# Kernel optimization log

Measured on AMD Instinct MI355X. Metric: run time of the kernel, lower is better.

The kernel has to match this reference:

```python
import jax, jax.numpy as jnp
import numpy as np

EPS = 1e-5
DIM = 1024

def layer_norm(x, gamma, beta):
    mu = jnp.mean(x, axis=-1, keepdims=True)
    var = jnp.var(x, axis=-1, keepdims=True)
    return (x - mu) * jax.lax.rsqrt(var + EPS) * gamma + beta

def setup_inputs() -> dict:
    key = jax.random.key(0)
    k1, k2 = jax.random.split(key)
    return {
        "image_features": jax.random.normal(k1, (32, 1024, DIM), dtype=jnp.float32),
        "text_features": jax.random.normal(k2, (32, 512, DIM), dtype=jnp.float32),
        "gamma": jnp.ones((DIM,), dtype=jnp.float32),
        "beta": jnp.zeros((DIM,), dtype=jnp.float32),
    }

def reference(image_features, text_features, gamma, beta):
    scale = DIM ** (-0.5)
    image_norm = layer_norm(image_features, gamma, beta)   # [B, Ni, D]
    text_norm = layer_norm(text_features, gamma, beta)     # [B, Nt, D]
    # shared attention matrix, softmax only over text axis
    attn = jax.nn.softmax(jnp.einsum('bid,btd->bit', image_norm, text_norm) * scale, axis=-1)  # [B, Ni, Nt]
    image_attended = jnp.einsum('bit,btd->bid', attn, text_norm)   # [B, Ni, D]
    text_attended = jnp.einsum('bit,bid->btd', attn, image_norm)   # [B, Nt, D] (attn reused transposed, no re-softmax)
    return (image_features + image_attended, text_features + text_attended)
```

## Files before the change

### kernel.cpp

```cpp
#include <hip/hip_runtime.h>
#include <hip/hip_bf16.h>

#define B_  32
#define NI_ 1024
#define NT_ 512
#define D_  1024

typedef __attribute__((ext_vector_type(8))) short bf16x8;
typedef __attribute__((ext_vector_type(4))) float f32x4;

__device__ __forceinline__ ushort f2b(float f) {
  unsigned u = __builtin_bit_cast(unsigned, f);
  u = (u + 0x7FFFu + ((u >> 16) & 1u)) >> 16;
  return (ushort)u;
}

__global__ __launch_bounds__(256) void ln_bf16_kernel(
    const float* __restrict__ x, const float* __restrict__ gamma,
    const float* __restrict__ beta, ushort* __restrict__ out)
{
  const int row  = blockIdx.x * 4 + (threadIdx.x >> 6);
  const int lane = threadIdx.x & 63;
  const float* xr = x + (size_t)row * D_;
  float4 v[4];
  float s = 0.f, sq = 0.f;
#pragma unroll
  for (int q = 0; q < 4; ++q) {
    v[q] = *reinterpret_cast<const float4*>(xr + q * 256 + lane * 4);
    s  += v[q].x + v[q].y + v[q].z + v[q].w;
    sq += v[q].x*v[q].x + v[q].y*v[q].y + v[q].z*v[q].z + v[q].w*v[q].w;
  }
#pragma unroll
  for (int m = 1; m < 64; m <<= 1) {
    s  += __shfl_xor(s,  m);
    sq += __shfl_xor(sq, m);
  }
  const float mean = s * (1.f / D_);
  const float rstd = rsqrtf(sq * (1.f / D_) - mean * mean + 1e-5f);
  ushort* orow = out + (size_t)row * D_;
#pragma unroll
  for (int q = 0; q < 4; ++q) {
    const float4 g  = *reinterpret_cast<const float4*>(gamma + q * 256 + lane * 4);
    const float4 bt = *reinterpret_cast<const float4*>(beta  + q * 256 + lane * 4);
    ushort4 o;
    o.x = f2b((v[q].x - mean) * rstd * g.x + bt.x);
    o.y = f2b((v[q].y - mean) * rstd * g.y + bt.y);
    o.z = f2b((v[q].z - mean) * rstd * g.z + bt.z);
    o.w = f2b((v[q].w - mean) * rstd * g.w + bt.w);
    *reinterpret_cast<ushort4*>(orow + q * 256 + lane * 4) = o;
  }
}

__global__ __launch_bounds__(256) void transpose_bf16_kernel(
    const ushort* __restrict__ in, ushort* __restrict__ out, int R, int C)
{
  __shared__ ushort lds[64][68];
  const size_t nb = (size_t)blockIdx.z * (size_t)R * C;
  const ushort* ib = in + nb;
  ushort* ob = out + nb;
  const int c0 = blockIdx.x * 64, r0 = blockIdx.y * 64;
  const int t = threadIdx.x;
#pragma unroll
  for (int it = 0; it < 2; ++it) {
    const int r = (t >> 3) + 32 * it;
    const int c = (t & 7) * 8;
    uint4 val = *reinterpret_cast<const uint4*>(ib + (size_t)(r0 + r) * C + c0 + c);
    *reinterpret_cast<uint2*>(&lds[r][c])     = make_uint2(val.x, val.y);
    *reinterpret_cast<uint2*>(&lds[r][c + 4]) = make_uint2(val.z, val.w);
  }
  __syncthreads();
#pragma unroll
  for (int it = 0; it < 2; ++it) {
    const int c  = (t >> 3) + 32 * it;
    const int rb = (t & 7) * 8;
    union { ushort u[8]; uint4 v; } pk;
#pragma unroll
    for (int j = 0; j < 8; ++j) pk.u[j] = lds[rb + j][c];
    *reinterpret_cast<uint4*>(ob + (size_t)(c0 + c) * R + r0 + rb) = pk.v;
  }
}

__global__ __launch_bounds__(512) void qk_softmax_kernel(
    const ushort* __restrict__ qn,
    const ushort* __restrict__ kn,
    ushort* __restrict__ attn_it,
    ushort* __restrict__ attn_ti)
{
  __shared__ __align__(16) ushort Asm[2][64 * 32];
  __shared__ __align__(16) ushort Bsm[2][512 * 32];
  __shared__ __align__(16) float redm[64][8];
  __shared__ __align__(16) float reds[64][8];

  const int bid = blockIdx.x;
  const int sid = (bid & 7) * 64 + (bid >> 3);
  const int b   = sid >> 4;
  const int i0  = (sid & 15) * 64;
  const int tid  = threadIdx.x;
  const int w    = tid >> 6;
  const int lane = tid & 63;
  const int lr   = lane & 15;
  const int g    = lane >> 4;

  const ushort* qb = qn + ((size_t)b * NI_ + i0) * D_;
  const ushort* kb = kn + (size_t)b * NT_ * D_;

  const int srow = tid >> 2;
  const int scol = (tid & 3) * 8;

  uint4 ra, rb0, rb1, rb2, rb3;
  auto LOAD = [&](int t) {
    const int ko = t * 32 + scol;
    if (tid < 256) ra = *reinterpret_cast<const uint4*>(qb + (size_t)srow * D_ + ko);
    rb0 = *reinterpret_cast<const uint4*>(kb + (size_t)(srow      ) * D_ + ko);
    rb1 = *reinterpret_cast<const uint4*>(kb + (size_t)(srow + 128) * D_ + ko);
    rb2 = *reinterpret_cast<const uint4*>(kb + (size_t)(srow + 256) * D_ + ko);
    rb3 = *reinterpret_cast<const uint4*>(kb + (size_t)(srow + 384) * D_ + ko);
  };
  auto WRITE = [&](int nb) {
    if (tid < 256) *reinterpret_cast<uint4*>(&Asm[nb][tid * 8]) = ra;
    *reinterpret_cast<uint4*>(&Bsm[nb][tid * 8        ]) = rb0;
    *reinterpret_cast<uint4*>(&Bsm[nb][tid * 8 +  4096]) = rb1;
    *reinterpret_cast<uint4*>(&Bsm[nb][tid * 8 +  8192]) = rb2;
    *reinterpret_cast<uint4*>(&Bsm[nb][tid * 8 + 12288]) = rb3;
  };

  f32x4 acc[4][4];
#pragma unroll
  for (int i = 0; i < 4; ++i)
#pragma unroll
    for (int j = 0; j < 4; ++j) acc[i][j] = (f32x4){0.f, 0.f, 0.f, 0.f};

  LOAD(0); WRITE(0); __syncthreads();
  const int nst = D_ / 32;
  int cur = 0;
  for (int t = 0; t < nst; ++t) {
    if (t + 1 < nst) LOAD(t + 1);
    const ushort* As = Asm[cur];
    const ushort* Bs = Bsm[cur];
    bf16x8 af[4], bf[4];
#pragma unroll
    for (int i = 0; i < 4; ++i)
      af[i] = *reinterpret_cast<const bf16x8*>(As + i * 512 + lr * 32 + g * 8);
#pragma unroll
    for (int j = 0; j < 4; ++j)
      bf[j] = *reinterpret_cast<const bf16x8*>(Bs + w * 2048 + j * 512 + lr * 32 + g * 8);
#pragma unroll
    for (int i = 0; i < 4; ++i)
#pragma unroll
      for (int j = 0; j < 4; ++j)
        acc[i][j] = __builtin_amdgcn_mfma_f32_16x16x32_bf16(af[i], bf[j], acc[i][j], 0, 0, 0);
    __syncthreads();
    if (t + 1 < nst) WRITE(cur ^ 1);
    __syncthreads();
    cur ^= 1;
  }

  const float c1 = 0.03125f * 1.44269504f;

  float mx[4][4];
#pragma unroll
  for (int i = 0; i < 4; ++i)
#pragma unroll
    for (int r = 0; r < 4; ++r) {
      float m = fmaxf(fmaxf(acc[i][0][r], acc[i][1][r]),
                      fmaxf(acc[i][2][r], acc[i][3][r]));
      m = fmaxf(m, __shfl_xor(m, 1));
      m = fmaxf(m, __shfl_xor(m, 2));
      m = fmaxf(m, __shfl_xor(m, 4));
      m = fmaxf(m, __shfl_xor(m, 8));
      mx[i][r] = m;
    }
  if (lr == 0) {
#pragma unroll
    for (int i = 0; i < 4; ++i)
#pragma unroll
      for (int r = 0; r < 4; ++r) redm[i * 16 + g * 4 + r][w] = mx[i][r];
  }
  __syncthreads();
  float gm[4][4];
#pragma unroll
  for (int i = 0; i < 4; ++i)
#pragma unroll
    for (int r = 0; r < 4; ++r) {
      const int row = i * 16 + g * 4 + r;
      const float4 a0 = *reinterpret_cast<const float4*>(&redm[row][0]);
      const float4 a1 = *reinterpret_cast<const float4*>(&redm[row][4]);
      gm[i][r] = fmaxf(fmaxf(fmaxf(a0.x, a0.y), fmaxf(a0.z, a0.w)),
                       fmaxf(fmaxf(a1.x, a1.y), fmaxf(a1.z, a1.w)));
    }

  float sm[4][4];
#pragma unroll
  for (int i = 0; i < 4; ++i)
#pragma unroll
    for (int r = 0; r < 4; ++r) sm[i][r] = 0.f;
#pragma unroll
  for (int i = 0; i < 4; ++i)
#pragma unroll
    for (int j = 0; j < 4; ++j)
#pragma unroll
      for (int r = 0; r < 4; ++r) {
        const float p = exp2f((acc[i][j][r] - gm[i][r]) * c1);
        acc[i][j][r] = p;
        sm[i][r] += p;
      }
#pragma unroll
  for (int i = 0; i < 4; ++i)
#pragma unroll
    for (int r = 0; r < 4; ++r) {
      float s = sm[i][r];
      s += __shfl_xor(s, 1);
      s += __shfl_xor(s, 2);
      s += __shfl_xor(s, 4);
      s += __shfl_xor(s, 8);
      sm[i][r] = s;
    }
  if (lr == 0) {
#pragma unroll
    for (int i = 0; i < 4; ++i)
#pragma unroll
      for (int r = 0; r < 4; ++r) reds[i * 16 + g * 4 + r][w] = sm[i][r];
  }
  __syncthreads();
  float inv[4][4];
#pragma unroll
  for (int i = 0; i < 4; ++i)
#pragma unroll
    for (int r = 0; r < 4; ++r) {
      const int row = i * 16 + g * 4 + r;
      const float4 a0 = *reinterpret_cast<const float4*>(&reds[row][0]);
      const float4 a1 = *reinterpret_cast<const float4*>(&reds[row][4]);
      inv[i][r] = 1.f / (a0.x + a0.y + a0.z + a0.w + a1.x + a1.y + a1.z + a1.w);
    }

#pragma unroll
  for (int i = 0; i < 4; ++i) {
    const int rbase = i0 + i * 16 + g * 4;
#pragma unroll
    for (int j = 0; j < 4; ++j) {
      const int tcol = w * 64 + j * 16 + lr;
      ushort4 pk;
      pk.x = f2b(acc[i][j][0] * inv[i][0]);
      pk.y = f2b(acc[i][j][1] * inv[i][1]);
      pk.z = f2b(acc[i][j][2] * inv[i][2]);
      pk.w = f2b(acc[i][j][3] * inv[i][3]);
      ushort* it_p = attn_it + ((size_t)b * NI_ + rbase) * NT_ + tcol;
      it_p[0 * NT_] = pk.x;
      it_p[1 * NT_] = pk.y;
      it_p[2 * NT_] = pk.z;
      it_p[3 * NT_] = pk.w;
      *reinterpret_cast<ushort4*>(attn_ti + ((size_t)b * NT_ + tcol) * NI_ + rbase) = pk;
    }
  }
}

__global__ __launch_bounds__(256) void bt_gemm_add_kernel(
    const ushort* __restrict__ A,
    const ushort* __restrict__ Bm,
    const float* __restrict__ add,
    float* __restrict__ out,
    int M, int N, int K)
{
  __shared__ __align__(16) ushort Asm[2][128 * 32];
  __shared__ __align__(16) ushort Bsm[2][128 * 32];

  const int b    = blockIdx.z;
  const int m0   = blockIdx.y * 128;
  const int n0   = blockIdx.x * 128;
  const int tid  = threadIdx.x;
  const int w    = tid >> 6;
  const int lane = tid & 63;
  const int lr   = lane & 15;
  const int g    = lane >> 4;
  const int wm   = (w >> 1) * 64;
  const int wn   = (w & 1) * 64;

  const ushort* Ab = A  + ((size_t)b * M + m0) * K;
  const ushort* Bb = Bm + ((size_t)b * N + n0) * K;

  const int srow = tid >> 2;
  const int scol = (tid & 3) * 8;

  uint4 ra0, ra1, rbx0, rbx1;
  auto LOAD = [&](int t) {
    const int ko = t * 32 + scol;
    ra0  = *reinterpret_cast<const uint4*>(Ab + (size_t)(srow     ) * K + ko);
    ra1  = *reinterpret_cast<const uint4*>(Ab + (size_t)(srow + 64) * K + ko);
    rbx0 = *reinterpret_cast<const uint4*>(Bb + (size_t)(srow     ) * K + ko);
    rbx1 = *reinterpret_cast<const uint4*>(Bb + (size_t)(srow + 64) * K + ko);
  };
  auto WRITE = [&](int nb) {
    *reinterpret_cast<uint4*>(&Asm[nb][tid * 8       ]) = ra0;
    *reinterpret_cast<uint4*>(&Asm[nb][tid * 8 + 2048]) = ra1;
    *reinterpret_cast<uint4*>(&Bsm[nb][tid * 8       ]) = rbx0;
    *reinterpret_cast<uint4*>(&Bsm[nb][tid * 8 + 2048]) = rbx1;
  };

  f32x4 acc[4][4];
#pragma unroll
  for (int i = 0; i < 4; ++i)
#pragma unroll
    for (int j = 0; j < 4; ++j) acc[i][j] = (f32x4){0.f, 0.f, 0.f, 0.f};

  LOAD(0); WRITE(0); __syncthreads();
  const int nst = K / 32;
  int cur = 0;
  for (int t = 0; t < nst; ++t) {
    if (t + 1 < nst) LOAD(t + 1);
    const ushort* As = Asm[cur];
    const ushort* Bs = Bsm[cur];
    bf16x8 af[4], bf[4];
#pragma unroll
    for (int i = 0; i < 4; ++i)
      af[i] = *reinterpret_cast<const bf16x8*>(As + (wm + i * 16 + lr) * 32 + g * 8);
#pragma unroll
    for (int j = 0; j < 4; ++j)
      bf[j] = *reinterpret_cast<const bf16x8*>(Bs + (wn + j * 16 + lr) * 32 + g * 8);
#pragma unroll
    for (int i = 0; i < 4; ++i)
#pragma unroll
      for (int j = 0; j < 4; ++j)
        acc[i][j] = __builtin_amdgcn_mfma_f32_16x16x32_bf16(af[i], bf[j], acc[i][j], 0, 0, 0);
    __syncthreads();
    if (t + 1 < nst) WRITE(cur ^ 1);
    __syncthreads();
    cur ^= 1;
  }

  const size_t ob = (size_t)b * M * N;
  const int rbase = m0 + wm + g * 4;
#pragma unroll
  for (int i = 0; i < 4; ++i)
#pragma unroll
    for (int j = 0; j < 4; ++j) {
      const int c = n0 + wn + j * 16 + lr;
#pragma unroll
      for (int r = 0; r < 4; ++r) {
        const size_t idx = ob + (size_t)(rbase + i * 16 + r) * N + c;
        out[idx] = add[idx] + acc[i][j][r];
      }
    }
}

extern "C" void kernel_launch(void* const* d_in, const int* in_sizes, int n_in,
                              void* d_out, int out_size, void* d_ws, size_t ws_size,
                              hipStream_t stream) {
  const float* imgf  = (const float*)d_in[0];
  const float* txtf  = (const float*)d_in[1];
  const float* gamma = (const float*)d_in[2];
  const float* beta  = (const float*)d_in[3];

  float* out0 = (float*)d_out;
  float* out1 = out0 + (size_t)B_ * NI_ * D_;

  const size_t SZ = (size_t)B_ * NT_ * NI_ * 2;
  char* ws = (char*)d_ws;
  ushort* attn_ti = (ushort*)ws;
  ushort* attn_it = (ushort*)(ws + SZ);
  ushort* txnT    = (ushort*)(ws + 2 * SZ);
  ushort* imnT    = (ushort*)(ws + SZ);
  ushort* imn     = (ushort*)out1;
  ushort* txn     = (ushort*)out0;

  ln_bf16_kernel<<<(B_ * NI_) / 4, 256, 0, stream>>>(imgf, gamma, beta, imn);
  ln_bf16_kernel<<<(B_ * NT_) / 4, 256, 0, stream>>>(txtf, gamma, beta, txn);
  qk_softmax_kernel<<<(NI_ / 64) * B_, 512, 0, stream>>>(imn, txn, attn_it, attn_ti);
  transpose_bf16_kernel<<<dim3(D_ / 64, NT_ / 64, B_), 256, 0, stream>>>(txn, txnT, NT_, D_);
  bt_gemm_add_kernel<<<dim3(D_ / 128, NI_ / 128, B_), 256, 0, stream>>>(
      attn_it, txnT, imgf, out0, NI_, D_, NT_);
  transpose_bf16_kernel<<<dim3(D_ / 64, NI_ / 64, B_), 256, 0, stream>>>(imn, imnT, NI_, D_);
  bt_gemm_add_kernel<<<dim3(D_ / 128, NT_ / 128, B_), 256, 0, stream>>>(
      attn_ti, imnT, txtf, out1, NT_, D_, NI_);
}
```

Baseline: 336.1 us.

## Use direct global-to-LDS loads for GEMM tile staging and drop one barrier

```diff
diff --git a/kernel.cpp b/kernel.cpp
--- a/kernel.cpp
+++ b/kernel.cpp
@@ -13,6 +13,12 @@
   unsigned u = __builtin_bit_cast(unsigned, f);
   u = (u + 0x7FFFu + ((u >> 16) & 1u)) >> 16;
   return (ushort)u;
+}
+
+__device__ __forceinline__ void gll16(const ushort* g, ushort* l) {
+  __builtin_amdgcn_global_load_lds(
+      (const __attribute__((address_space(1))) void*)g,
+      (__attribute__((address_space(3))) void*)l, 16, 0, 0);
 }
 
 __global__ __launch_bounds__(256) void ln_bf16_kernel(
@@ -104,25 +110,20 @@
   const ushort* qb = qn + ((size_t)b * NI_ + i0) * D_;
   const ushort* kb = kn + (size_t)b * NT_ * D_;
 
-  const int srow = tid >> 2;
-  const int scol = (tid & 3) * 8;
-
-  uint4 ra, rb0, rb1, rb2, rb3;
-  auto LOAD = [&](int t) {
-    const int ko = t * 32 + scol;
-    if (tid < 256) ra = *reinterpret_cast<const uint4*>(qb + (size_t)srow * D_ + ko);
-    rb0 = *reinterpret_cast<const uint4*>(kb + (size_t)(srow      ) * D_ + ko);
-    rb1 = *reinterpret_cast<const uint4*>(kb + (size_t)(srow + 128) * D_ + ko);
-    rb2 = *reinterpret_cast<const uint4*>(kb + (size_t)(srow + 256) * D_ + ko);
-    rb3 = *reinterpret_cast<const uint4*>(kb + (size_t)(srow + 384) * D_ + ko);
+  auto ISSUE = [&](int nb, int t) {
+    const int ko = t * 32;
+#pragma unroll
+    for (int q = 0; q < 4; ++q) {
+      const int c = q * 512 + w * 64 + lane;
+      gll16(kb + (size_t)(c >> 2) * D_ + ko + (c & 3) * 8,
+            &Bsm[nb][(q * 512 + w * 64) * 8]);
+    }
+    if (w < 4) {
+      const int c = w * 64 + lane;
+      gll16(qb + (size_t)(c >> 2) * D_ + ko + (c & 3) * 8,
+            &Asm[nb][(w * 64) * 8]);
+    }
   };
-  auto WRITE = [&](int nb) {
-    if (tid < 256) *reinterpret_cast<uint4*>(&Asm[nb][tid * 8]) = ra;
-    *reinterpret_cast<uint4*>(&Bsm[nb][tid * 8        ]) = rb0;
-    *reinterpret_cast<uint4*>(&Bsm[nb][tid * 8 +  4096]) = rb1;
-    *reinterpret_cast<uint4*>(&Bsm[nb][tid * 8 +  8192]) = rb2;
-    *reinterpret_cast<uint4*>(&Bsm[nb][tid * 8 + 12288]) = rb3;
-  };
 
   f32x4 acc[4][4];
 #pragma unroll
@@ -130,11 +131,12 @@
 #pragma unroll
     for (int j = 0; j < 4; ++j) acc[i][j] = (f32x4){0.f, 0.f, 0.f, 0.f};
 
-  LOAD(0); WRITE(0); __syncthreads();
+  ISSUE(0, 0);
+  __syncthreads();
   const int nst = D_ / 32;
   int cur = 0;
   for (int t = 0; t < nst; ++t) {
-    if (t + 1 < nst) LOAD(t + 1);
+    if (t + 1 < nst) ISSUE(cur ^ 1, t + 1);
     const ushort* As = Asm[cur];
     const ushort* Bs = Bsm[cur];
     bf16x8 af[4], bf[4];
@@ -149,8 +151,6 @@
 #pragma unroll
       for (int j = 0; j < 4; ++j)
         acc[i][j] = __builtin_amdgcn_mfma_f32_16x16x32_bf16(af[i], bf[j], acc[i][j], 0, 0, 0);
-    __syncthreads();
-    if (t + 1 < nst) WRITE(cur ^ 1);
     __syncthreads();
     cur ^= 1;
   }
@@ -278,23 +278,17 @@
   const ushort* Ab = A  + ((size_t)b * M + m0) * K;
   const ushort* Bb = Bm + ((size_t)b * N + n0) * K;
 
-  const int srow = tid >> 2;
-  const int scol = (tid & 3) * 8;
-
-  uint4 ra0, ra1, rbx0, rbx1;
-  auto LOAD = [&](int t) {
-    const int ko = t * 32 + scol;
-    ra0  = *reinterpret_cast<const uint4*>(Ab + (size_t)(srow     ) * K + ko);
-    ra1  = *reinterpret_cast<const uint4*>(Ab + (size_t)(srow + 64) * K + ko);
-    rbx0 = *reinterpret_cast<const uint4*>(Bb + (size_t)(srow     ) * K + ko);
-    rbx1 = *reinterpret_cast<const uint4*>(Bb + (size_t)(srow + 64) * K + ko);
+  auto ISSUE = [&](int nb, int t) {
+    const int ko = t * 32;
+#pragma unroll
+    for (int q = 0; q < 2; ++q) {
+      const int c = q * 256 + w * 64 + lane;
+      const size_t go = (size_t)(c >> 2) * K + ko + (c & 3) * 8;
+      const int lo = (q * 256 + w * 64) * 8;
+      gll16(Ab + go, &Asm[nb][lo]);
+      gll16(Bb + go, &Bsm[nb][lo]);
+    }
   };
-  auto WRITE = [&](int nb) {
-    *reinterpret_cast<uint4*>(&Asm[nb][tid * 8       ]) = ra0;
-    *reinterpret_cast<uint4*>(&Asm[nb][tid * 8 + 2048]) = ra1;
-    *reinterpret_cast<uint4*>(&Bsm[nb][tid * 8       ]) = rbx0;
-    *reinterpret_cast<uint4*>(&Bsm[nb][tid * 8 + 2048]) = rbx1;
-  };
 
   f32x4 acc[4][4];
 #pragma unroll
@@ -302,11 +296,12 @@
 #pragma unroll
     for (int j = 0; j < 4; ++j) acc[i][j] = (f32x4){0.f, 0.f, 0.f, 0.f};
 
-  LOAD(0); WRITE(0); __syncthreads();
+  ISSUE(0, 0);
+  __syncthreads();
   const int nst = K / 32;
   int cur = 0;
   for (int t = 0; t < nst; ++t) {
-    if (t + 1 < nst) LOAD(t + 1);
+    if (t + 1 < nst) ISSUE(cur ^ 1, t + 1);
     const ushort* As = Asm[cur];
     const ushort* Bs = Bsm[cur];
     bf16x8 af[4], bf[4];
@@ -321,8 +316,6 @@
 #pragma unroll
       for (int j = 0; j < 4; ++j)
         acc[i][j] = __builtin_amdgcn_mfma_f32_16x16x32_bf16(af[i], bf[j], acc[i][j], 0, 0, 0);
-    __syncthreads();
-    if (t + 1 < nst) WRITE(cur ^ 1);
     __syncthreads();
     cur ^= 1;
   }
```

Result: slower. 363.0 us (+8.0%).

## Swizzle LDS tiles and add two-stage register prefetch in GEMM kernels

Applied to the files above, without the earlier changes.

```diff
diff --git a/kernel.cpp b/kernel.cpp
--- a/kernel.cpp
+++ b/kernel.cpp
@@ -14,6 +14,7 @@
   u = (u + 0x7FFFu + ((u >> 16) & 1u)) >> 16;
   return (ushort)u;
 }
+
 
 __global__ __launch_bounds__(256) void ln_bf16_kernel(
     const float* __restrict__ x, const float* __restrict__ gamma,
@@ -106,22 +107,27 @@
 
   const int srow = tid >> 2;
   const int scol = (tid & 3) * 8;
-
-  uint4 ra, rb0, rb1, rb2, rb3;
-  auto LOAD = [&](int t) {
+  const int wpos = ((tid >> 6) << 6) | (((tid >> 2) & 15) << 2)
+                 | ((tid & 3) ^ ((tid >> 3) & 3));
+  const int chunkLane = ((lane & 15) << 2) | ((lane >> 4) ^ ((lane >> 1) & 3));
+
+  struct QT { uint4 a, b0, b1, b2, b3; };
+  QT rA, rB;
+  auto LOAD = [&](int t, QT& r) {
     const int ko = t * 32 + scol;
-    if (tid < 256) ra = *reinterpret_cast<const uint4*>(qb + (size_t)srow * D_ + ko);
-    rb0 = *reinterpret_cast<const uint4*>(kb + (size_t)(srow      ) * D_ + ko);
-    rb1 = *reinterpret_cast<const uint4*>(kb + (size_t)(srow + 128) * D_ + ko);
-    rb2 = *reinterpret_cast<const uint4*>(kb + (size_t)(srow + 256) * D_ + ko);
-    rb3 = *reinterpret_cast<const uint4*>(kb + (size_t)(srow + 384) * D_ + ko);
-  };
-  auto WRITE = [&](int nb) {
-    if (tid < 256) *reinterpret_cast<uint4*>(&Asm[nb][tid * 8]) = ra;
-    *reinterpret_cast<uint4*>(&Bsm[nb][tid * 8        ]) = rb0;
-    *reinterpret_cast<uint4*>(&Bsm[nb][tid * 8 +  4096]) = rb1;
-    *reinterpret_cast<uint4*>(&Bsm[nb][tid * 8 +  8192]) = rb2;
-    *reinterpret_cast<uint4*>(&Bsm[nb][tid * 8 + 12288]) = rb3;
+    if (tid < 256) r.a = *reinterpret_cast<const uint4*>(qb + (size_t)srow * D_ + ko);
+    r.b0 = *reinterpret_cast<const uint4*>(kb + (size_t)(srow      ) * D_ + ko);
+    r.b1 = *reinterpret_cast<const uint4*>(kb + (size_t)(srow + 128) * D_ + ko);
+    r.b2 = *reinterpret_cast<const uint4*>(kb + (size_t)(srow + 256) * D_ + ko);
+    r.b3 = *reinterpret_cast<const uint4*>(kb + (size_t)(srow + 384) * D_ + ko);
+  };
+  auto WRITE = [&](int nb, QT& r) {
+    const int wp = wpos * 8;
+    if (tid < 256) *reinterpret_cast<uint4*>(&Asm[nb][wp]) = r.a;
+    *reinterpret_cast<uint4*>(&Bsm[nb][wp         ]) = r.b0;
+    *reinterpret_cast<uint4*>(&Bsm[nb][wp +  4096 ]) = r.b1;
+    *reinterpret_cast<uint4*>(&Bsm[nb][wp +  8192 ]) = r.b2;
+    *reinterpret_cast<uint4*>(&Bsm[nb][wp + 12288 ]) = r.b3;
   };
 
   f32x4 acc[4][4];
@@ -130,29 +136,38 @@
 #pragma unroll
     for (int j = 0; j < 4; ++j) acc[i][j] = (f32x4){0.f, 0.f, 0.f, 0.f};
 
-  LOAD(0); WRITE(0); __syncthreads();
-  const int nst = D_ / 32;
-  int cur = 0;
-  for (int t = 0; t < nst; ++t) {
-    if (t + 1 < nst) LOAD(t + 1);
-    const ushort* As = Asm[cur];
-    const ushort* Bs = Bsm[cur];
+  auto MFMA = [&](int nb) {
+    const ushort* As = Asm[nb];
+    const ushort* Bs = Bsm[nb];
     bf16x8 af[4], bf[4];
 #pragma unroll
     for (int i = 0; i < 4; ++i)
-      af[i] = *reinterpret_cast<const bf16x8*>(As + i * 512 + lr * 32 + g * 8);
+      af[i] = *reinterpret_cast<const bf16x8*>(As + (i * 64 + chunkLane) * 8);
 #pragma unroll
     for (int j = 0; j < 4; ++j)
-      bf[j] = *reinterpret_cast<const bf16x8*>(Bs + w * 2048 + j * 512 + lr * 32 + g * 8);
+      bf[j] = *reinterpret_cast<const bf16x8*>(Bs + (((w * 4 + j) * 64 + chunkLane)) * 8);
 #pragma unroll
     for (int i = 0; i < 4; ++i)
 #pragma unroll
       for (int j = 0; j < 4; ++j)
         acc[i][j] = __builtin_amdgcn_mfma_f32_16x16x32_bf16(af[i], bf[j], acc[i][j], 0, 0, 0);
-    __syncthreads();
-    if (t + 1 < nst) WRITE(cur ^ 1);
-    __syncthreads();
-    cur ^= 1;
+  };
+
+  const int nst = D_ / 32;
+  LOAD(0, rA); WRITE(0, rA);
+  LOAD(1, rB);
+  __syncthreads();
+  for (int t = 0; t < nst; t += 2) {
+    if (t + 2 < nst) LOAD(t + 2, rA);
+    MFMA(0);
+    __syncthreads();
+    WRITE(1, rB);
+    __syncthreads();
+    if (t + 3 < nst) LOAD(t + 3, rB);
+    MFMA(1);
+    __syncthreads();
+    if (t + 2 < nst) WRITE(0, rA);
+    __syncthreads();
   }
 
   const float c1 = 0.03125f * 1.44269504f;
@@ -272,28 +287,31 @@
   const int lane = tid & 63;
   const int lr   = lane & 15;
   const int g    = lane >> 4;
-  const int wm   = (w >> 1) * 64;
-  const int wn   = (w & 1) * 64;
 
   const ushort* Ab = A  + ((size_t)b * M + m0) * K;
   const ushort* Bb = Bm + ((size_t)b * N + n0) * K;
 
   const int srow = tid >> 2;
   const int scol = (tid & 3) * 8;
-
-  uint4 ra0, ra1, rbx0, rbx1;
-  auto LOAD = [&](int t) {
+  const int wpos = ((tid >> 6) << 6) | (((tid >> 2) & 15) << 2)
+                 | ((tid & 3) ^ ((tid >> 3) & 3));
+  const int chunkLane = ((lane & 15) << 2) | ((lane >> 4) ^ ((lane >> 1) & 3));
+
+  struct GT { uint4 a0, a1, b0, b1; };
+  GT rA, rB;
+  auto LOAD = [&](int t, GT& r) {
     const int ko = t * 32 + scol;
-    ra0  = *reinterpret_cast<const uint4*>(Ab + (size_t)(srow     ) * K + ko);
-    ra1  = *reinterpret_cast<const uint4*>(Ab + (size_t)(srow + 64) * K + ko);
-    rbx0 = *reinterpret_cast<const uint4*>(Bb + (size_t)(srow     ) * K + ko);
-    rbx1 = *reinterpret_cast<const uint4*>(Bb + (size_t)(srow + 64) * K + ko);
-  };
-  auto WRITE = [&](int nb) {
-    *reinterpret_cast<uint4*>(&Asm[nb][tid * 8       ]) = ra0;
-    *reinterpret_cast<uint4*>(&Asm[nb][tid * 8 + 2048]) = ra1;
-    *reinterpret_cast<uint4*>(&Bsm[nb][tid * 8       ]) = rbx0;
-    *reinterpret_cast<uint4*>(&Bsm[nb][tid * 8 + 2048]) = rbx1;
+    r.a0 = *reinterpret_cast<const uint4*>(Ab + (size_t)(srow     ) * K + ko);
+    r.a1 = *reinterpret_cast<const uint4*>(Ab + (size_t)(srow + 64) * K + ko);
+    r.b0 = *reinterpret_cast<const uint4*>(Bb + (size_t)(srow     ) * K + ko);
+    r.b1 = *reinterpret_cast<const uint4*>(Bb + (size_t)(srow + 64) * K + ko);
+  };
+  auto WRITE = [&](int nb, GT& r) {
+    const int wp = wpos * 8;
+    *reinterpret_cast<uint4*>(&Asm[nb][wp       ]) = r.a0;
+    *reinterpret_cast<uint4*>(&Asm[nb][wp + 2048]) = r.a1;
+    *reinterpret_cast<uint4*>(&Bsm[nb][wp       ]) = r.b0;
+    *reinterpret_cast<uint4*>(&Bsm[nb][wp + 2048]) = r.b1;
   };
 
   f32x4 acc[4][4];
@@ -302,38 +320,49 @@
 #pragma unroll
     for (int j = 0; j < 4; ++j) acc[i][j] = (f32x4){0.f, 0.f, 0.f, 0.f};
 
-  LOAD(0); WRITE(0); __syncthreads();
-  const int nst = K / 32;
-  int cur = 0;
-  for (int t = 0; t < nst; ++t) {
-    if (t + 1 < nst) LOAD(t + 1);
-    const ushort* As = Asm[cur];
-    const ushort* Bs = Bsm[cur];
+  auto MFMA = [&](int nb) {
+    const ushort* As = Asm[nb];
+    const ushort* Bs = Bsm[nb];
     bf16x8 af[4], bf[4];
 #pragma unroll
     for (int i = 0; i < 4; ++i)
-      af[i] = *reinterpret_cast<const bf16x8*>(As + (wm + i * 16 + lr) * 32 + g * 8);
+      af[i] = *reinterpret_cast<const bf16x8*>(
+          As + ((((w >> 1) * 4 + i) * 64 + chunkLane)) * 8);
 #pragma unroll
     for (int j = 0; j < 4; ++j)
-      bf[j] = *reinterpret_cast<const bf16x8*>(Bs + (wn + j * 16 + lr) * 32 + g * 8);
+      bf[j] = *reinterpret_cast<const bf16x8*>(
+          Bs + ((((w & 1) * 4 + j) * 64 + chunkLane)) * 8);
 #pragma unroll
     for (int i = 0; i < 4; ++i)
 #pragma unroll
       for (int j = 0; j < 4; ++j)
         acc[i][j] = __builtin_amdgcn_mfma_f32_16x16x32_bf16(af[i], bf[j], acc[i][j], 0, 0, 0);
-    __syncthreads();
-    if (t + 1 < nst) WRITE(cur ^ 1);
-    __syncthreads();
-    cur ^= 1;
+  };
+
+  const int nst = K / 32;
+  LOAD(0, rA); WRITE(0, rA);
+  LOAD(1, rB);
+  __syncthreads();
+  for (int t = 0; t < nst; t += 2) {
+    if (t + 2 < nst) LOAD(t + 2, rA);
+    MFMA(0);
+    __syncthreads();
+    WRITE(1, rB);
+    __syncthreads();
+    if (t + 3 < nst) LOAD(t + 3, rB);
+    MFMA(1);
+    __syncthreads();
+    if (t + 2 < nst) WRITE(0, rA);
+    __syncthreads();
   }
 
   const size_t ob = (size_t)b * M * N;
-  const int rbase = m0 + wm + g * 4;
+  const int rbase = m0 + (w >> 1) * 64 + g * 4;
 #pragma unroll
   for (int i = 0; i < 4; ++i)
 #pragma unroll
     for (int j = 0; j < 4; ++j) {
-      const int c = n0 + wn + j * 16 + lr;
+      const int c = n0 + (w & 1) * 64 + j * 16 + lr;
 #pragma unroll
       for (int r = 0; r < 4; ++r) {
         const size_t idx = ob + (size_t)(rbase + i * 16 + r) * N + c;
```

Measured after the change: 790.6 us. +135.2%, slower.
